# Kernel optimization log

Hardware: AMD Instinct MI355X
Metric: run time of the kernel (lower is better)

## Reference

```python
import jax, jax.numpy as jnp
import numpy as np

B, N, D = 4, 4096, 1024
STD = 1.0 / D

def setup_inputs() -> dict:
    key = jax.random.key(0)
    ks = jax.random.split(key, 6)
    return {
        "x_real": jax.random.normal(ks[0], (B, N, D), dtype=jnp.float32),
        "x_imag": jax.random.normal(ks[1], (B, N, D), dtype=jnp.float32),
        "w_query_real": jax.random.normal(ks[2], (D, D), dtype=jnp.float32) * STD,
        "w_query_imag": jax.random.normal(ks[3], (D, D), dtype=jnp.float32) * STD,
        "w_key": jax.random.normal(ks[4], (D, D), dtype=jnp.float32) * STD,
        "w_value": jax.random.normal(ks[5], (D, D), dtype=jnp.float32) * STD,
    }

def reference(x_real, x_imag, w_query_real, w_query_imag, w_key, w_value):
    # query gate: (x.real @ Wqr) * (x.imag @ Wqi)  -> [b, n, e]
    query = jnp.einsum('bnd,de->bne', x_real, w_query_real) * \
            jnp.einsum('bnd,de->bne', x_imag, w_query_imag)
    key = jnp.einsum('bnd,de->bne', x_real, w_key)      # [b, n, d]
    value = jnp.einsum('bnd,de->bne', x_imag, w_value)  # [b, n, e]
    # linear-attention style reduction over sequence dim n
    kv_attn = jnp.einsum('bnd,bne->bde', key, value)    # [b, d, e]
    # dropout with p=0.0 (eval / identity)
    bffn = jnp.einsum('bnd,bde->bne', query, kv_attn)   # [b, n, e]
    return bffn
```

## Files before the change

kernel.cpp:

```cpp
#include <hip/hip_runtime.h>
#include <stdint.h>

typedef unsigned short ushort_t;
typedef __attribute__((ext_vector_type(8))) short bf16x8;
typedef __attribute__((ext_vector_type(4))) float f32x4;

__device__ __forceinline__ ushort_t f2bf(float f) {
  union { float f; uint32_t u; } v; v.f = f;
  uint32_t u = v.u;
  u += 0x7FFFu + ((u >> 16) & 1u);
  return (ushort_t)(u >> 16);
}
__device__ __forceinline__ float bf2f(ushort_t h) {
  union { uint32_t u; float f; } v; v.u = ((uint32_t)h) << 16;
  return v.f;
}
__device__ __forceinline__ void gl2lds16(const void* g, void* l) {
  __builtin_amdgcn_global_load_lds(
      (__attribute__((address_space(1))) void*)(uintptr_t)g,
      (__attribute__((address_space(3))) void*)(uint32_t)(uintptr_t)l,
      16, 0, 0);
}

__device__ __forceinline__ void gemm256(
    const ushort_t* __restrict__ A, int lda,
    const ushort_t* __restrict__ Bt, int ldb,
    int m0, int n0, int K, char* __restrict__ smem,
    f32x4 (&acc)[8][4]) {
  const int t = threadIdx.x;
  const int lane = t & 63, wid = t >> 6;
  const int wm = wid >> 2, wn = wid & 3;
  const int lr = lane & 15, lq = lane >> 4;
  const int nt = K >> 6;

  const int row0 = t >> 3, row1 = (512 + t) >> 3;
  const int kg0 = (t & 7) ^ (row0 & 7), kg1 = (t & 7) ^ (row1 & 7);
  const ushort_t* a0 = A + (size_t)(m0 + row0) * lda + kg0 * 8;
  const ushort_t* a1 = A + (size_t)(m0 + row1) * lda + kg1 * 8;
  const ushort_t* b0 = Bt + (size_t)(n0 + row0) * ldb + kg0 * 8;
  const ushort_t* b1 = Bt + (size_t)(n0 + row1) * ldb + kg1 * 8;
  const int d0 = t * 16, d1 = (512 + t) * 16;

  const int o0 = lr * 128 + ((lq ^ (lr & 7)) << 4);
  const int o1 = lr * 128 + (((4 + lq) ^ (lr & 7)) << 4);
  const char* aB = smem + wm * 16384;
  const char* bB = smem + 65536 + wn * 8192;

#define STG_A(tt, h, buf) do { if ((tt) < nt) { \
    gl2lds16(a0 + (h) * 128 * lda + (tt) * 64, smem + (buf) * 32768 + (h) * 16384 + d0); \
    gl2lds16(a1 + (h) * 128 * lda + (tt) * 64, smem + (buf) * 32768 + (h) * 16384 + d1); } } while (0)
#define STG_B(tt, h, buf) do { if ((tt) < nt) { \
    gl2lds16(b0 + (h) * 128 * ldb + (tt) * 64, smem + 65536 + (buf) * 32768 + (h) * 16384 + d0); \
    gl2lds16(b1 + (h) * 128 * ldb + (tt) * 64, smem + 65536 + (buf) * 32768 + (h) * 16384 + d1); } } while (0)
#define AF_(buf, mig, s) (*(const bf16x8*)(aB + (buf) * 32768 + (mig) * 2048 + o##s))
#define BF_(buf, nig, s) (*(const bf16x8*)(bB + (buf) * 32768 + (nig) * 2048 + o##s))
#define MFMA16(AR, M0, N0) \
    __builtin_amdgcn_s_setprio(1); \
    _Pragma("unroll") \
    for (int mi = 0; mi < 4; ++mi) \
      _Pragma("unroll") \
      for (int ni = 0; ni < 2; ++ni) { \
        acc[(M0) + mi][(N0) + ni] = __builtin_amdgcn_mfma_f32_16x16x32_bf16(AR[mi][0], bF[ni][0], acc[(M0) + mi][(N0) + ni], 0, 0, 0); \
        acc[(M0) + mi][(N0) + ni] = __builtin_amdgcn_mfma_f32_16x16x32_bf16(AR[mi][1], bF[ni][1], acc[(M0) + mi][(N0) + ni], 0, 0, 0); \
      } \
    __builtin_amdgcn_s_setprio(0);

  bf16x8 aLo[4][2], aHi[4][2], bF[2][2];

  STG_A(0, 0, 0); STG_A(0, 1, 0); STG_B(0, 0, 0); STG_B(0, 1, 0);
  STG_A(1, 0, 1); STG_A(1, 1, 1);
  asm volatile("s_waitcnt vmcnt(4)" ::: "memory");
  __builtin_amdgcn_s_barrier();

  const int niter = nt >> 1;
  for (int i = 0; i < niter; ++i) {
    const int t2 = 2 * i + 2, t3 = 2 * i + 3;
    #pragma unroll
    for (int mi = 0; mi < 4; ++mi) { aLo[mi][0] = AF_(0, mi, 0); aLo[mi][1] = AF_(0, mi, 1); }
    #pragma unroll
    for (int ni = 0; ni < 2; ++ni) { bF[ni][0] = BF_(0, ni, 0); bF[ni][1] = BF_(0, ni, 1); }
    STG_B(2 * i + 1, 0, 1);
    __builtin_amdgcn_s_barrier();
    MFMA16(aLo, 0, 0)
    __builtin_amdgcn_s_barrier();
    #pragma unroll
    for (int mi = 0; mi < 4; ++mi) { aHi[mi][0] = AF_(0, 4 + mi, 0); aHi[mi][1] = AF_(0, 4 + mi, 1); }
    STG_B(2 * i + 1, 1, 1);
    __builtin_amdgcn_s_barrier();
    MFMA16(aHi, 4, 0)
    __builtin_amdgcn_s_barrier();
    #pragma unroll
    for (int ni = 0; ni < 2; ++ni) { bF[ni][0] = BF_(0, 2 + ni, 0); bF[ni][1] = BF_(0, 2 + ni, 1); }
    STG_A(t2, 0, 0);
    __builtin_amdgcn_s_barrier();
    MFMA16(aLo, 0, 2)
    __builtin_amdgcn_s_barrier();
    STG_A(t2, 1, 0);
    __builtin_amdgcn_s_barrier();
    MFMA16(aHi, 4, 2)
    asm volatile("s_waitcnt vmcnt(4)" ::: "memory");
    __builtin_amdgcn_s_barrier();
    #pragma unroll
    for (int mi = 0; mi < 4; ++mi) { aLo[mi][0] = AF_(1, mi, 0); aLo[mi][1] = AF_(1, mi, 1); }
    #pragma unroll
    for (int ni = 0; ni < 2; ++ni) { bF[ni][0] = BF_(1, ni, 0); bF[ni][1] = BF_(1, ni, 1); }
    STG_B(t2, 0, 0);
    __builtin_amdgcn_s_barrier();
    MFMA16(aLo, 0, 0)
    __builtin_amdgcn_s_barrier();
    #pragma unroll
    for (int mi = 0; mi < 4; ++mi) { aHi[mi][0] = AF_(1, 4 + mi, 0); aHi[mi][1] = AF_(1, 4 + mi, 1); }
    STG_B(t2, 1, 0);
    __builtin_amdgcn_s_barrier();
    MFMA16(aHi, 4, 0)
    __builtin_amdgcn_s_barrier();
    #pragma unroll
    for (int ni = 0; ni < 2; ++ni) { bF[ni][0] = BF_(1, 2 + ni, 0); bF[ni][1] = BF_(1, 2 + ni, 1); }
    STG_A(t3, 0, 1);
    __builtin_amdgcn_s_barrier();
    MFMA16(aLo, 0, 2)
    __builtin_amdgcn_s_barrier();
    STG_A(t3, 1, 1);
    __builtin_amdgcn_s_barrier();
    MFMA16(aHi, 4, 2)
    asm volatile("s_waitcnt vmcnt(4)" ::: "memory");
    __builtin_amdgcn_s_barrier();
  }
#undef STG_A
#undef STG_B
#undef AF_
#undef BF_
#undef MFMA16
}

template <bool GATE>
__global__ __launch_bounds__(512, 2) void proj8(
    const ushort_t* __restrict__ X, const ushort_t* __restrict__ Wt,
    ushort_t* __restrict__ Cq, ushort_t* __restrict__ Ct,
    const ushort_t* __restrict__ gate) {
  extern __shared__ char smem[];
  const int bid = blockIdx.x;
  const int xcd = bid & 7, i = bid >> 3;
  const int m0 = (xcd * 8 + (i >> 3)) * 256;
  const int n0 = (i & 7) * 256;
  f32x4 acc[8][4] = {};
  gemm256(X, 1024, Wt, 1024, m0, n0, 1024, smem, acc);

  const int t = threadIdx.x, lane = t & 63, wid = t >> 6;
  const int wm = wid >> 2, wn = wid & 3;
  const int lr = lane & 15, lq = lane >> 4;

  if (n0 < 1024) {
    #pragma unroll
    for (int mi = 0; mi < 8; ++mi) {
      int rbase = m0 + wm * 128 + mi * 16 + lq * 4;
      #pragma unroll
      for (int ni = 0; ni < 4; ++ni) {
        int c = n0 + wn * 64 + ni * 16 + lr;
        #pragma unroll
        for (int r = 0; r < 4; ++r) {
          float v = acc[mi][ni][r];
          if constexpr (GATE) v *= bf2f(gate[(size_t)(rbase + r) * 1024 + c]);
          Cq[(size_t)(rbase + r) * 1024 + c] = f2bf(v);
        }
      }
    }
  } else {
    __syncthreads();
    #pragma unroll
    for (int mi = 0; mi < 8; ++mi) {
      int ns0 = wm * 128 + mi * 16 + lq * 4;
      int nc = ns0 >> 3, half8 = (ns0 >> 2) & 1;
      #pragma unroll
      for (int ni = 0; ni < 4; ++ni) {
        int dl = wn * 64 + ni * 16 + lr;
        ushort4 u = make_ushort4(f2bf(acc[mi][ni][0]), f2bf(acc[mi][ni][1]),
                                 f2bf(acc[mi][ni][2]), f2bf(acc[mi][ni][3]));
        *(ushort4*)(smem + dl * 512 + ((nc ^ (dl & 31)) * 16) + half8 * 8) = u;
      }
    }
    __syncthreads();
    const int b = m0 >> 12, nseq0 = m0 & 4095;
    #pragma unroll
    for (int j = 0; j < 16; ++j) {
      int g = j * 512 + t;
      int dl = g >> 5, nc = g & 31;
      bf16x8 v = *(const bf16x8*)(smem + dl * 512 + ((nc ^ (dl & 31)) * 16));
      int d = n0 - 1024 + dl;
      *(bf16x8*)&Ct[(((size_t)(b * 1024 + d)) << 12) + nseq0 + nc * 8] = v;
    }
  }
}

__global__ __launch_bounds__(512, 2) void kv8(
    const ushort_t* __restrict__ VT, const ushort_t* __restrict__ KT,
    ushort_t* __restrict__ P) {
  extern __shared__ char smem[];
  const int bid = blockIdx.x;
  const int xcd = bid & 7, i = bid >> 3;
  const int z = xcd * 2 + (i >> 4);
  const int mn = i & 15;
  const int m0 = (mn >> 2) * 256, n0 = (mn & 3) * 256;
  const int b = z & 3, s = z >> 2;
  const ushort_t* A = VT + ((size_t)b << 22) + s * 1024;
  const ushort_t* Bt = KT + ((size_t)b << 22) + s * 1024;
  f32x4 acc[8][4] = {};
  gemm256(A, 4096, Bt, 4096, m0, n0, 1024, smem, acc);

  const int t = threadIdx.x, lane = t & 63, wid = t >> 6;
  const int wm = wid >> 2, wn = wid & 3;
  const int lr = lane & 15, lq = lane >> 4;
  ushort_t* C = P + ((size_t)z << 20);
  #pragma unroll
  for (int mi = 0; mi < 8; ++mi) {
    int rbase = m0 + wm * 128 + mi * 16 + lq * 4;
    #pragma unroll
    for (int ni = 0; ni < 4; ++ni) {
      int c = n0 + wn * 64 + ni * 16 + lr;
      #pragma unroll
      for (int r = 0; r < 4; ++r)
        C[(size_t)(rbase + r) * 1024 + c] = f2bf(acc[mi][ni][r]);
    }
  }
}

__global__ __launch_bounds__(256) void kv_reduce(const ushort_t* __restrict__ P,
                                                 ushort_t* __restrict__ KVT) {
  size_t e4 = ((size_t)blockIdx.x * 256 + threadIdx.x) * 4;
  int b = (int)(e4 >> 20);
  size_t j = e4 & ((1u << 20) - 1);
  float s0 = 0.f, s1 = 0.f, s2 = 0.f, s3 = 0.f;
  #pragma unroll
  for (int sp = 0; sp < 4; ++sp) {
    ushort4 v = *(const ushort4*)(P + ((size_t)(sp * 4 + b) << 20) + j);
    s0 += bf2f(v.x); s1 += bf2f(v.y); s2 += bf2f(v.z); s3 += bf2f(v.w);
  }
  *(ushort4*)&KVT[e4] = make_ushort4(f2bf(s0), f2bf(s1), f2bf(s2), f2bf(s3));
}

__global__ __launch_bounds__(512, 2) void fin8(
    const ushort_t* __restrict__ Q, const ushort_t* __restrict__ KVT,
    float* __restrict__ Out) {
  extern __shared__ char smem[];
  const int bid = blockIdx.x;
  const int xcd = bid & 7, i = bid >> 3;
  const int m0 = (xcd * 8 + (i >> 2)) * 256;
  const int n0 = (i & 3) * 256;
  const int b = m0 >> 12;
  f32x4 acc[8][4] = {};
  gemm256(Q, 1024, KVT + ((size_t)b << 20), 1024, m0, n0, 1024, smem, acc);

  const int t = threadIdx.x, lane = t & 63, wid = t >> 6;
  const int wm = wid >> 2, wn = wid & 3;
  const int lr = lane & 15, lq = lane >> 4;
  #pragma unroll
  for (int mi = 0; mi < 8; ++mi) {
    int rbase = m0 + wm * 128 + mi * 16 + lq * 4;
    #pragma unroll
    for (int ni = 0; ni < 4; ++ni) {
      int c = n0 + wn * 64 + ni * 16 + lr;
      #pragma unroll
      for (int r = 0; r < 4; ++r)
        Out[(size_t)(rbase + r) * 1024 + c] = acc[mi][ni][r];
    }
  }
}

__global__ __launch_bounds__(256) void prep(
    const float* __restrict__ xr, const float* __restrict__ xi,
    const float* w0, const float* w1, const float* w2, const float* w3,
    ushort_t* __restrict__ xrb, ushort_t* __restrict__ xib,
    ushort_t* o0, ushort_t* o1, ushort_t* o2, ushort_t* o3) {
  const int bid = blockIdx.x;
  const int t = threadIdx.x;
  if (bid < 4096) {
    __shared__ float tile[32][33];
    const float* W; ushort_t* O;
    switch (bid >> 10) {
      case 0: W = w0; O = o0; break;
      case 1: W = w1; O = o1; break;
      case 2: W = w2; O = o2; break;
      default: W = w3; O = o3; break;
    }
    const int within = bid & 1023;
    const int bx = (within & 31) * 32, by = (within >> 5) * 32;
    const int tx = t & 31, ty = t >> 5;
    #pragma unroll
    for (int k = 0; k < 32; k += 8)
      tile[ty + k][tx] = W[(size_t)(by + ty + k) * 1024 + bx + tx];
    __syncthreads();
    #pragma unroll
    for (int k = 0; k < 32; k += 8)
      O[(size_t)(bx + ty + k) * 1024 + by + tx] = f2bf(tile[tx][ty + k]);
  } else {
    const size_t T = 16u * 1024u * 1024u;
    size_t e = ((size_t)(bid - 4096) * 256 + t) * 8;
    const float* src; ushort_t* dst;
    if (e < T) { src = xr + e; dst = xrb + e; }
    else       { src = xi + (e - T); dst = xib + (e - T); }
    float4 f0 = *(const float4*)src;
    float4 f1 = *(const float4*)(src + 4);
    ushort4 u0 = make_ushort4(f2bf(f0.x), f2bf(f0.y), f2bf(f0.z), f2bf(f0.w));
    ushort4 u1 = make_ushort4(f2bf(f1.x), f2bf(f1.y), f2bf(f1.z), f2bf(f1.w));
    *(ushort4*)dst = u0;
    *(ushort4*)(dst + 4) = u1;
  }
}

extern "C" void kernel_launch(void* const* d_in, const int* in_sizes, int n_in,
                              void* d_out, int out_size, void* d_ws, size_t ws_size,
                              hipStream_t stream) {
  const float* xr  = (const float*)d_in[0];
  const float* xi  = (const float*)d_in[1];
  const float* wqr = (const float*)d_in[2];
  const float* wqi = (const float*)d_in[3];
  const float* wk  = (const float*)d_in[4];
  const float* wv  = (const float*)d_in[5];

  char* ws = (char*)d_ws;
  const size_t MB = 1024ull * 1024ull;
  ushort_t* WtQR = (ushort_t*)(ws + 0 * MB);
  ushort_t* WtK  = (ushort_t*)(ws + 2 * MB);
  ushort_t* WtQI = (ushort_t*)(ws + 4 * MB);
  ushort_t* WtV  = (ushort_t*)(ws + 6 * MB);
  ushort_t* Xrb  = (ushort_t*)(ws + 8 * MB);
  ushort_t* Xib  = (ushort_t*)(ws + 40 * MB);
  ushort_t* KT   = (ushort_t*)(ws + 72 * MB);
  ushort_t* Q    = (ushort_t*)(ws + 104 * MB);
  ushort_t* VT   = (ushort_t*)(ws + 8 * MB);
  ushort_t* KVT  = (ushort_t*)(ws + 40 * MB);
  ushort_t* QR   = (ushort_t*)d_out;
  ushort_t* KVP  = (ushort_t*)d_out;

  static bool inited = false;
  if (!inited) {
    inited = true;
    hipFuncSetAttribute((const void*)&proj8<false>, hipFuncAttributeMaxDynamicSharedMemorySize, 131072);
    hipFuncSetAttribute((const void*)&proj8<true>,  hipFuncAttributeMaxDynamicSharedMemorySize, 131072);
    hipFuncSetAttribute((const void*)&kv8,          hipFuncAttributeMaxDynamicSharedMemorySize, 131072);
    hipFuncSetAttribute((const void*)&fin8,         hipFuncAttributeMaxDynamicSharedMemorySize, 131072);
  }

  prep<<<20480, 256, 0, stream>>>(xr, xi, wqr, wqi, wk, wv,
                                  Xrb, Xib, WtQR, WtQI, WtK, WtV);
  proj8<false><<<512, 512, 131072, stream>>>(Xrb, WtQR, QR, KT, nullptr);
  proj8<true><<<512, 512, 131072, stream>>>(Xib, WtQI, Q, VT, QR);
  kv8<<<256, 512, 131072, stream>>>(VT, KT, KVP);
  kv_reduce<<<4096, 256, 0, stream>>>(KVP, KVT);
  fin8<<<256, 512, 131072, stream>>>(Q, KVT, (float*)d_out);
}
```

Baseline: 402.6 us.

## Replace 8-phase ping-pong GEMM pipeline with simple double-buffered per-tile loop

Swaps the hand-scheduled, barrier-heavy 8-phase loop (interleaving A/B half-tile stages with MFMA groups) for a plain double-buffered loop. Each iteration waits for all loads, issues a single barrier, prefetches the next full K-tile, then loads fragments and runs four MFMA groups. This cuts the number of barriers and simplifies the schedule. In exchange it gives up fine-grained overlap of global loads with compute and holds more B fragments in registers.

```diff
diff --git a/kernel.cpp b/kernel.cpp
--- a/kernel.cpp
+++ b/kernel.cpp
@@ -40,96 +40,65 @@
   const ushort_t* b0 = Bt + (size_t)(n0 + row0) * ldb + kg0 * 8;
   const ushort_t* b1 = Bt + (size_t)(n0 + row1) * ldb + kg1 * 8;
   const int d0 = t * 16, d1 = (512 + t) * 16;
+  const int ldaT = 128 * lda, ldbT = 128 * ldb;
 
   const int o0 = lr * 128 + ((lq ^ (lr & 7)) << 4);
   const int o1 = lr * 128 + (((4 + lq) ^ (lr & 7)) << 4);
   const char* aB = smem + wm * 16384;
   const char* bB = smem + 65536 + wn * 8192;
 
-#define STG_A(tt, h, buf) do { if ((tt) < nt) { \
-    gl2lds16(a0 + (h) * 128 * lda + (tt) * 64, smem + (buf) * 32768 + (h) * 16384 + d0); \
-    gl2lds16(a1 + (h) * 128 * lda + (tt) * 64, smem + (buf) * 32768 + (h) * 16384 + d1); } } while (0)
-#define STG_B(tt, h, buf) do { if ((tt) < nt) { \
-    gl2lds16(b0 + (h) * 128 * ldb + (tt) * 64, smem + 65536 + (buf) * 32768 + (h) * 16384 + d0); \
-    gl2lds16(b1 + (h) * 128 * ldb + (tt) * 64, smem + 65536 + (buf) * 32768 + (h) * 16384 + d1); } } while (0)
-#define AF_(buf, mig, s) (*(const bf16x8*)(aB + (buf) * 32768 + (mig) * 2048 + o##s))
-#define BF_(buf, nig, s) (*(const bf16x8*)(bB + (buf) * 32768 + (nig) * 2048 + o##s))
-#define MFMA16(AR, M0, N0) \
+#define STAGE_TILE(tt, nb) do { \
+    char* sA = smem + (nb); char* sB = smem + 65536 + (nb); \
+    const ushort_t* ga0 = a0 + (tt) * 64; const ushort_t* ga1 = a1 + (tt) * 64; \
+    const ushort_t* gb0 = b0 + (tt) * 64; const ushort_t* gb1 = b1 + (tt) * 64; \
+    gl2lds16(ga0, sA + d0); gl2lds16(ga1, sA + d1); \
+    gl2lds16(ga0 + ldaT, sA + 16384 + d0); gl2lds16(ga1 + ldaT, sA + 16384 + d1); \
+    gl2lds16(gb0, sB + d0); gl2lds16(gb1, sB + d1); \
+    gl2lds16(gb0 + ldbT, sB + 16384 + d0); gl2lds16(gb1 + ldbT, sB + 16384 + d1); \
+  } while (0)
+
+#define MFMA16(NOFF, MOFF) \
     __builtin_amdgcn_s_setprio(1); \
     _Pragma("unroll") \
     for (int mi = 0; mi < 4; ++mi) \
       _Pragma("unroll") \
       for (int ni = 0; ni < 2; ++ni) { \
-        acc[(M0) + mi][(N0) + ni] = __builtin_amdgcn_mfma_f32_16x16x32_bf16(AR[mi][0], bF[ni][0], acc[(M0) + mi][(N0) + ni], 0, 0, 0); \
-        acc[(M0) + mi][(N0) + ni] = __builtin_amdgcn_mfma_f32_16x16x32_bf16(AR[mi][1], bF[ni][1], acc[(M0) + mi][(N0) + ni], 0, 0, 0); \
+        acc[(MOFF) + mi][(NOFF) + ni] = __builtin_amdgcn_mfma_f32_16x16x32_bf16(aF[mi][0], bF[(NOFF) + ni][0], acc[(MOFF) + mi][(NOFF) + ni], 0, 0, 0); \
+        acc[(MOFF) + mi][(NOFF) + ni] = __builtin_amdgcn_mfma_f32_16x16x32_bf16(aF[mi][1], bF[(NOFF) + ni][1], acc[(MOFF) + mi][(NOFF) + ni], 0, 0, 0); \
       } \
     __builtin_amdgcn_s_setprio(0);
 
-  bf16x8 aLo[4][2], aHi[4][2], bF[2][2];
-
-  STG_A(0, 0, 0); STG_A(0, 1, 0); STG_B(0, 0, 0); STG_B(0, 1, 0);
-  STG_A(1, 0, 1); STG_A(1, 1, 1);
-  asm volatile("s_waitcnt vmcnt(4)" ::: "memory");
-  __builtin_amdgcn_s_barrier();
-
-  const int niter = nt >> 1;
-  for (int i = 0; i < niter; ++i) {
-    const int t2 = 2 * i + 2, t3 = 2 * i + 3;
-    #pragma unroll
-    for (int mi = 0; mi < 4; ++mi) { aLo[mi][0] = AF_(0, mi, 0); aLo[mi][1] = AF_(0, mi, 1); }
-    #pragma unroll
-    for (int ni = 0; ni < 2; ++ni) { bF[ni][0] = BF_(0, ni, 0); bF[ni][1] = BF_(0, ni, 1); }
-    STG_B(2 * i + 1, 0, 1);
-    __builtin_amdgcn_s_barrier();
-    MFMA16(aLo, 0, 0)
-    __builtin_amdgcn_s_barrier();
-    #pragma unroll
-    for (int mi = 0; mi < 4; ++mi) { aHi[mi][0] = AF_(0, 4 + mi, 0); aHi[mi][1] = AF_(0, 4 + mi, 1); }
-    STG_B(2 * i + 1, 1, 1);
-    __builtin_amdgcn_s_barrier();
-    MFMA16(aHi, 4, 0)
-    __builtin_amdgcn_s_barrier();
-    #pragma unroll
-    for (int ni = 0; ni < 2; ++ni) { bF[ni][0] = BF_(0, 2 + ni, 0); bF[ni][1] = BF_(0, 2 + ni, 1); }
-    STG_A(t2, 0, 0);
-    __builtin_amdgcn_s_barrier();
-    MFMA16(aLo, 0, 2)
-    __builtin_amdgcn_s_barrier();
-    STG_A(t2, 1, 0);
-    __builtin_amdgcn_s_barrier();
-    MFMA16(aHi, 4, 2)
-    asm volatile("s_waitcnt vmcnt(4)" ::: "memory");
-    __builtin_amdgcn_s_barrier();
-    #pragma unroll
-    for (int mi = 0; mi < 4; ++mi) { aLo[mi][0] = AF_(1, mi, 0); aLo[mi][1] = AF_(1, mi, 1); }
-    #pragma unroll
-    for (int ni = 0; ni < 2; ++ni) { bF[ni][0] = BF_(1, ni, 0); bF[ni][1] = BF_(1, ni, 1); }
-    STG_B(t2, 0, 0);
-    __builtin_amdgcn_s_barrier();
-    MFMA16(aLo, 0, 0)
-    __builtin_amdgcn_s_barrier();
-    #pragma unroll
-    for (int mi = 0; mi < 4; ++mi) { aHi[mi][0] = AF_(1, 4 + mi, 0); aHi[mi][1] = AF_(1, 4 + mi, 1); }
-    STG_B(t2, 1, 0);
-    __builtin_amdgcn_s_barrier();
-    MFMA16(aHi, 4, 0)
-    __builtin_amdgcn_s_barrier();
-    #pragma unroll
-    for (int ni = 0; ni < 2; ++ni) { bF[ni][0] = BF_(1, 2 + ni, 0); bF[ni][1] = BF_(1, 2 + ni, 1); }
-    STG_A(t3, 0, 1);
-    __builtin_amdgcn_s_barrier();
-    MFMA16(aLo, 0, 2)
-    __builtin_amdgcn_s_barrier();
-    STG_A(t3, 1, 1);
-    __builtin_amdgcn_s_barrier();
-    MFMA16(aHi, 4, 2)
-    asm volatile("s_waitcnt vmcnt(4)" ::: "memory");
-    __builtin_amdgcn_s_barrier();
-  }
-#undef STG_A
-#undef STG_B
-#undef AF_
-#undef BF_
+  bf16x8 aF[4][2], bF[4][2];
+
+  STAGE_TILE(0, 0);
+
+  for (int tt = 0; tt < nt; ++tt) {
+    asm volatile("s_waitcnt vmcnt(0) lgkmcnt(0)\n\ts_barrier" ::: "memory");
+    const int cb = (tt & 1) << 15;
+    if (tt + 1 < nt) STAGE_TILE(tt + 1, ((tt + 1) & 1) << 15);
+    const char* aP = aB + cb;
+    const char* bP = bB + cb;
+    #pragma unroll
+    for (int mi = 0; mi < 4; ++mi) {
+      aF[mi][0] = *(const bf16x8*)(aP + mi * 2048 + o0);
+      aF[mi][1] = *(const bf16x8*)(aP + mi * 2048 + o1);
+    }
+    #pragma unroll
+    for (int ni = 0; ni < 4; ++ni) {
+      bF[ni][0] = *(const bf16x8*)(bP + ni * 2048 + o0);
+      bF[ni][1] = *(const bf16x8*)(bP + ni * 2048 + o1);
+    }
+    MFMA16(0, 0)
+    MFMA16(2, 0)
+    #pragma unroll
+    for (int mi = 0; mi < 4; ++mi) {
+      aF[mi][0] = *(const bf16x8*)(aP + (4 + mi) * 2048 + o0);
+      aF[mi][1] = *(const bf16x8*)(aP + (4 + mi) * 2048 + o1);
+    }
+    MFMA16(0, 4)
+    MFMA16(2, 4)
+  }
+#undef STAGE_TILE
 #undef MFMA16
 }
 
```

New measurement: 399.3 us. Within noise of the previous version (-0.8%).
